# Performance work log

Measured on AMD Instinct MI355X. Metric: run time of the kernel, lower is better.

The kernel has to match this reference:

```python
import jax, jax.numpy as jnp
import numpy as np

B, T, V, H = 128, 256, 512, 1024
EOS_ID = 1


def _onehot_seq(key, eos_pos):
    k1, = jax.random.split(key, 1)
    toks = jax.random.randint(k1, (B, T), 2, V)  # avoid 0/1 so EOS only where planted
    toks = toks.at[jnp.arange(B), eos_pos].set(EOS_ID)
    return jax.nn.one_hot(toks, V, dtype=jnp.float32)


def setup_inputs() -> dict:
    key = jax.random.key(0)
    ks = jax.random.split(key, 12)
    enc_eos = jax.random.randint(ks[0], (B,), T // 2, T)
    dec_eos = jax.random.randint(ks[1], (B,), T // 2, T)
    s = 0.05
    return {
        "encoder_inputs": _onehot_seq(ks[2], enc_eos),
        "decoder_inputs": _onehot_seq(ks[3], dec_eos),
        "enc_Wi": jax.random.normal(ks[4], (V, 4 * H), jnp.float32) * s,
        "enc_Wh": jax.random.normal(ks[5], (H, 4 * H), jnp.float32) * s,
        "enc_b": jnp.zeros((4 * H,), jnp.float32),
        "dec_Wi": jax.random.normal(ks[6], (V, 4 * H), jnp.float32) * s,
        "dec_Wh": jax.random.normal(ks[7], (H, 4 * H), jnp.float32) * s,
        "dec_b": jnp.zeros((4 * H,), jnp.float32),
        "dense_W": jax.random.normal(ks[8], (H, V), jnp.float32) * s,
        "dense_b": jnp.zeros((V,), jnp.float32),
    }


def get_sequence_lengths(seq, eos_id=EOS_ID):
    eos_row = seq[:, :, eos_id]                      # [B,T]
    eos_idx = jnp.argmax(eos_row == eos_id, axis=-1)  # first position hitting EOS
    found = eos_row[jnp.arange(seq.shape[0]), eos_idx] == eos_id
    return jnp.where(found, eos_idx + 1, seq.shape[1])


def lstm_scan(c0, h0, x_btv, Wi, Wh, b):
    """Scans an LSTM over time axis 1; returns (c_seq, h_seq) each [B,T,H]."""
    def step(carry, x):
        c, h = carry
        z = x @ Wi + h @ Wh + b                      # [B,4H]
        i, f, g, o = jnp.split(z, 4, axis=-1)
        c = jax.nn.sigmoid(f) * c + jax.nn.sigmoid(i) * jnp.tanh(g)
        h = jax.nn.sigmoid(o) * jnp.tanh(c)
        return (c, h), (c, h)
    xs = jnp.swapaxes(x_btv, 0, 1)                   # [T,B,V]
    _, (cs, hs) = jax.lax.scan(step, (c0, h0), xs)
    return jnp.swapaxes(cs, 0, 1), jnp.swapaxes(hs, 0, 1)


def reference(encoder_inputs, decoder_inputs, enc_Wi, enc_Wh, enc_b,
              dec_Wi, dec_Wh, dec_b, dense_W, dense_b):
    b = encoder_inputs.shape[0]
    # --- encoder ---
    lengths = get_sequence_lengths(encoder_inputs)
    idx = jnp.maximum(0, lengths - 1)
    c0 = jnp.zeros((b, H), encoder_inputs.dtype)
    h0 = jnp.zeros((b, H), encoder_inputs.dtype)
    cs, hs = lstm_scan(c0, h0, encoder_inputs, enc_Wi, enc_Wh, enc_b)
    ar = jnp.arange(b)
    c_enc, h_enc = cs[ar, idx], hs[ar, idx]          # carry at EOS step
    # --- decoder (teacher forcing on decoder_inputs[:, :-1]) ---
    _, hd = lstm_scan(c_enc, h_enc, decoder_inputs[:, :-1], dec_Wi, dec_Wh, dec_b)
    logits = hd @ dense_W + dense_b                  # [B,T-1,V]
    return logits
```

## Files before the change

kernel.cpp:

```cpp
#include <hip/hip_runtime.h>

#define Bv 128
#define Tv 256
#define Vv 512
#define Hv 1024
#define FH 4096
#define TD 255

typedef unsigned short ushort_t;
typedef __attribute__((ext_vector_type(8))) short bf16x8;
typedef __attribute__((ext_vector_type(4))) float f32x4;

__device__ __forceinline__ ushort_t f2bf(float f) {
    unsigned u = __float_as_uint(f);
    unsigned r = (u + 0x7fffu + ((u >> 16) & 1u)) >> 16;
    return (ushort_t)r;
}
__device__ __forceinline__ float bf2f(ushort_t h) {
    return __uint_as_float(((unsigned)h) << 16);
}
__device__ __forceinline__ float sigm(float x) {
    return 1.0f / (1.0f + expf(-x));
}

__global__ __launch_bounds__(256) void wsplit_t(
    const float* __restrict__ W, int K, int N,
    ushort_t* __restrict__ hiT, ushort_t* __restrict__ loT)
{
    __shared__ float ts[32][65];
    const int n0 = blockIdx.x * 64, k0 = blockIdx.y * 32;
    const int tid = threadIdx.x;
#pragma unroll
    for (int i = 0; i < 8; i++) {
        int f = tid + i * 256;
        int k = f >> 6, nn = f & 63;
        ts[k][nn] = W[(size_t)(k0 + k) * N + n0 + nn];
    }
    __syncthreads();
#pragma unroll
    for (int i = 0; i < 8; i++) {
        int f = tid + i * 256;
        int nn = f >> 5, k = f & 31;
        float v = ts[k][nn];
        ushort_t h = f2bf(v);
        ushort_t l = f2bf(v - bf2f(h));
        size_t o = (size_t)(n0 + nn) * K + k0 + k;
        hiT[o] = h;
        loT[o] = l;
    }
}

__global__ __launch_bounds__(256) void extract_tokens(
    const float* __restrict__ x, int* __restrict__ tok)
{
    int row = blockIdx.x * 4 + (threadIdx.x >> 6);
    int lane = threadIdx.x & 63;
    const float* p = x + (size_t)row * Vv;
    int found = -1;
#pragma unroll
    for (int i = 0; i < 8; i++)
        if (p[lane + i * 64] > 0.5f) found = lane + i * 64;
#pragma unroll
    for (int off = 32; off > 0; off >>= 1) {
        int o = __shfl_down(found, off);
        found = found > o ? found : o;
    }
    if (lane == 0) tok[row] = found;
}

__global__ void find_eos(const int* __restrict__ tok, int* __restrict__ idx)
{
    int b = threadIdx.x;
    int first = Tv - 1;
    for (int t = Tv - 1; t >= 0; t--)
        if (tok[b * Tv + t] == 1) first = t;
    idx[b] = first;
}

__global__ __launch_bounds__(1024, 4) void lstm_step(
    const ushort_t* __restrict__ WhiT, const ushort_t* __restrict__ WloT,
    const float* __restrict__ Wi,
    const float* __restrict__ bias,
    const int* __restrict__ tok, int t,
    const ushort_t* __restrict__ hin_hi, const ushort_t* __restrict__ hin_lo,
    ushort_t* __restrict__ hout_hi, ushort_t* __restrict__ hout_lo,
    float* __restrict__ c_state,
    ushort_t* __restrict__ hex_hi, ushort_t* __restrict__ hex_lo,
    const int* __restrict__ save_idx,
    float* __restrict__ c_save, ushort_t* __restrict__ hs_hi, ushort_t* __restrict__ hs_lo)
{
    __shared__ float z_s[4][32][68];
    const int tid = threadIdx.x;
    const int wave = tid >> 6, lane = tid & 63;
    const int wk = wave >> 2;
    const int wm = wave & 1, wn = (wave >> 1) & 1;
    const int n = lane & 15, quad = lane >> 4;
    const int j0 = blockIdx.x * 16;
    const int b0 = blockIdx.y * 32;
    const int k0 = wk * 256;

    const bool act = tid < 512;
    const int bl = tid >> 4, jl = tid & 15;
    const int b_e = b0 + bl, col = j0 + jl;
    float w0 = 0.f, w1 = 0.f, w2 = 0.f, w3 = 0.f;
    float bz0 = 0.f, bz1 = 0.f, bz2 = 0.f, bz3 = 0.f;
    float c_old = 0.f;
    int sidx = -1;
    size_t off = 0;
    if (act) {
        int tk = tok[b_e * Tv + t];
        const float* wr = Wi + (size_t)tk * FH + col;
        w0 = wr[0]; w1 = wr[Hv]; w2 = wr[2 * Hv]; w3 = wr[3 * Hv];
        bz0 = bias[col];          bz1 = bias[Hv + col];
        bz2 = bias[2 * Hv + col]; bz3 = bias[3 * Hv + col];
        off = (size_t)b_e * Hv + col;
        c_old = c_state[off];
        if (save_idx) sidx = save_idx[b_e];
    }

    const size_t arow = (size_t)(b0 + wm * 16 + n) * Hv + k0 + quad * 8;
    const size_t g0 = (size_t)((2 * wn + 0) * Hv + j0 + n) * Hv + k0 + quad * 8;
    const size_t g1 = (size_t)((2 * wn + 1) * Hv + j0 + n) * Hv + k0 + quad * 8;

    f32x4 acc0 = {0.f, 0.f, 0.f, 0.f}, acc1 = {0.f, 0.f, 0.f, 0.f};

#pragma unroll 2
    for (int kc = 0; kc < 256; kc += 32) {
        bf16x8 ahi = *(const bf16x8*)(hin_hi + arow + kc);
        bf16x8 alo = *(const bf16x8*)(hin_lo + arow + kc);
        bf16x8 b0h = *(const bf16x8*)(WhiT + g0 + kc);
        bf16x8 b0l = *(const bf16x8*)(WloT + g0 + kc);
        bf16x8 b1h = *(const bf16x8*)(WhiT + g1 + kc);
        bf16x8 b1l = *(const bf16x8*)(WloT + g1 + kc);
        acc0 = __builtin_amdgcn_mfma_f32_16x16x32_bf16(ahi, b0h, acc0, 0, 0, 0);
        acc1 = __builtin_amdgcn_mfma_f32_16x16x32_bf16(ahi, b1h, acc1, 0, 0, 0);
        acc0 = __builtin_amdgcn_mfma_f32_16x16x32_bf16(alo, b0h, acc0, 0, 0, 0);
        acc1 = __builtin_amdgcn_mfma_f32_16x16x32_bf16(alo, b1h, acc1, 0, 0, 0);
        acc0 = __builtin_amdgcn_mfma_f32_16x16x32_bf16(ahi, b0l, acc0, 0, 0, 0);
        acc1 = __builtin_amdgcn_mfma_f32_16x16x32_bf16(ahi, b1l, acc1, 0, 0, 0);
    }

    const int row0 = wm * 16 + quad * 4;
    const int cb0 = (2 * wn + 0) * 16 + n;
    const int cb1 = cb0 + 16;
#pragma unroll
    for (int r = 0; r < 4; r++) {
        z_s[wk][row0 + r][cb0] = acc0[r];
        z_s[wk][row0 + r][cb1] = acc1[r];
    }
    __syncthreads();

    if (act) {
        float z0 = bz0 + w0, z1 = bz1 + w1, z2 = bz2 + w2, z3 = bz3 + w3;
#pragma unroll
        for (int q = 0; q < 4; q++) {
            z0 += z_s[q][bl][jl];
            z1 += z_s[q][bl][16 + jl];
            z2 += z_s[q][bl][32 + jl];
            z3 += z_s[q][bl][48 + jl];
        }
        float si = sigm(z0), sf = sigm(z1), so = sigm(z3);
        float gg = tanhf(z2);
        float cn = sf * c_old + si * gg;
        float hn = so * tanhf(cn);
        c_state[off] = cn;
        ushort_t hh = f2bf(hn);
        ushort_t hl = f2bf(hn - bf2f(hh));
        hout_hi[off] = hh;
        hout_lo[off] = hl;
        if (hex_hi) { hex_hi[off] = hh; hex_lo[off] = hl; }
        if (save_idx) {
            if (t == sidx) { c_save[off] = cn; hs_hi[off] = hh; hs_lo[off] = hl; }
        }
    }
}

__global__ __launch_bounds__(256) void dense_mfma(
    const ushort_t* __restrict__ Ahi, const ushort_t* __restrict__ Alo,
    const ushort_t* __restrict__ WhiT, const ushort_t* __restrict__ WloT,
    const float* __restrict__ bias, float* __restrict__ out)
{
    const int tid = threadIdx.x;
    const int wave = tid >> 6, lane = tid & 63;
    const int wm = wave & 1, wn = wave >> 1;
    const int n = lane & 15, quad = lane >> 4;
    const int m0 = blockIdx.y * 32 + wm * 16;
    const int c0 = blockIdx.x * 64 + wn * 32;

    const size_t arow = (size_t)(m0 + n) * Hv + quad * 8;
    const size_t g0 = (size_t)(c0 + 0 + n) * Hv + quad * 8;
    const size_t g1 = (size_t)(c0 + 16 + n) * Hv + quad * 8;

    f32x4 acc0 = {0.f, 0.f, 0.f, 0.f}, acc1 = {0.f, 0.f, 0.f, 0.f};

#pragma unroll 2
    for (int kc = 0; kc < Hv; kc += 32) {
        bf16x8 ahi = *(const bf16x8*)(Ahi + arow + kc);
        bf16x8 alo = *(const bf16x8*)(Alo + arow + kc);
        bf16x8 b0h = *(const bf16x8*)(WhiT + g0 + kc);
        bf16x8 b0l = *(const bf16x8*)(WloT + g0 + kc);
        bf16x8 b1h = *(const bf16x8*)(WhiT + g1 + kc);
        bf16x8 b1l = *(const bf16x8*)(WloT + g1 + kc);
        acc0 = __builtin_amdgcn_mfma_f32_16x16x32_bf16(ahi, b0h, acc0, 0, 0, 0);
        acc1 = __builtin_amdgcn_mfma_f32_16x16x32_bf16(ahi, b1h, acc1, 0, 0, 0);
        acc0 = __builtin_amdgcn_mfma_f32_16x16x32_bf16(alo, b0h, acc0, 0, 0, 0);
        acc1 = __builtin_amdgcn_mfma_f32_16x16x32_bf16(alo, b1h, acc1, 0, 0, 0);
        acc0 = __builtin_amdgcn_mfma_f32_16x16x32_bf16(ahi, b0l, acc0, 0, 0, 0);
        acc1 = __builtin_amdgcn_mfma_f32_16x16x32_bf16(ahi, b1l, acc1, 0, 0, 0);
    }

#pragma unroll
    for (int r = 0; r < 4; r++) {
        int row = m0 + quad * 4 + r;
        int tt = row >> 7, bb = row & 127;
        size_t o = ((size_t)bb * TD + tt) * Vv;
        int col0 = c0 + n, col1 = c0 + 16 + n;
        out[o + col0] = acc0[r] + bias[col0];
        out[o + col1] = acc1[r] + bias[col1];
    }
}

extern "C" void kernel_launch(void* const* d_in, const int* in_sizes, int n_in,
                              void* d_out, int out_size, void* d_ws, size_t ws_size,
                              hipStream_t stream)
{
    const float* enc_in  = (const float*)d_in[0];
    const float* dec_in  = (const float*)d_in[1];
    const float* enc_Wi  = (const float*)d_in[2];
    const float* enc_Wh  = (const float*)d_in[3];
    const float* enc_b   = (const float*)d_in[4];
    const float* dec_Wi  = (const float*)d_in[5];
    const float* dec_Wh  = (const float*)d_in[6];
    const float* dec_b   = (const float*)d_in[7];
    const float* dense_W = (const float*)d_in[8];
    const float* dense_b = (const float*)d_in[9];
    float* out = (float*)d_out;

    char* wp = (char*)d_ws;
    auto take = [&](size_t bytes) -> char* {
        char* p = wp;
        wp += (bytes + 255) & ~(size_t)255;
        return p;
    };

    ushort_t* hd_hi = (ushort_t*)take((size_t)TD * Bv * Hv * 2);
    ushort_t* hd_lo = (ushort_t*)take((size_t)TD * Bv * Hv * 2);
    ushort_t* eWhi  = (ushort_t*)take((size_t)FH * Hv * 2);
    ushort_t* eWlo  = (ushort_t*)take((size_t)FH * Hv * 2);
    ushort_t* dWhi  = (ushort_t*)take((size_t)FH * Hv * 2);
    ushort_t* dWlo  = (ushort_t*)take((size_t)FH * Hv * 2);
    ushort_t* nWhi  = (ushort_t*)take((size_t)Vv * Hv * 2);
    ushort_t* nWlo  = (ushort_t*)take((size_t)Vv * Hv * 2);
    ushort_t* hbh0  = (ushort_t*)take((size_t)Bv * Hv * 2);
    ushort_t* hbl0  = (ushort_t*)take((size_t)Bv * Hv * 2);
    ushort_t* hbh1  = (ushort_t*)take((size_t)Bv * Hv * 2);
    ushort_t* hbl1  = (ushort_t*)take((size_t)Bv * Hv * 2);
    ushort_t* hshi  = (ushort_t*)take((size_t)Bv * Hv * 2);
    ushort_t* hslo  = (ushort_t*)take((size_t)Bv * Hv * 2);
    float*    c_state = (float*)take((size_t)Bv * Hv * 4);
    float*    c_save  = (float*)take((size_t)Bv * Hv * 4);
    int*      etok  = (int*)take((size_t)Bv * Tv * 4);
    int*      dtok  = (int*)take((size_t)Bv * Tv * 4);
    int*      eidx  = (int*)take((size_t)Bv * 4);

    ushort_t* hbh[2] = {hbh0, hbh1};
    ushort_t* hbl[2] = {hbl0, hbl1};

    wsplit_t<<<dim3(FH / 64, Hv / 32), 256, 0, stream>>>(enc_Wh, Hv, FH, eWhi, eWlo);
    wsplit_t<<<dim3(FH / 64, Hv / 32), 256, 0, stream>>>(dec_Wh, Hv, FH, dWhi, dWlo);
    wsplit_t<<<dim3(Vv / 64, Hv / 32), 256, 0, stream>>>(dense_W, Hv, Vv, nWhi, nWlo);
    extract_tokens<<<Bv * Tv / 4, 256, 0, stream>>>(enc_in, etok);
    extract_tokens<<<Bv * Tv / 4, 256, 0, stream>>>(dec_in, dtok);
    find_eos<<<1, Bv, 0, stream>>>(etok, eidx);

    hipMemsetAsync(hbh0, 0, (size_t)Bv * Hv * 2, stream);
    hipMemsetAsync(hbl0, 0, (size_t)Bv * Hv * 2, stream);
    hipMemsetAsync(c_state, 0, (size_t)Bv * Hv * 4, stream);

    for (int t = 0; t < Tv; t++) {
        lstm_step<<<dim3(64, 4), 1024, 0, stream>>>(
            eWhi, eWlo, enc_Wi, enc_b, etok, t,
            hbh[t & 1], hbl[t & 1], hbh[(t + 1) & 1], hbl[(t + 1) & 1],
            c_state, nullptr, nullptr, eidx, c_save, hshi, hslo);
    }

    hipMemcpyAsync(c_state, c_save, (size_t)Bv * Hv * 4, hipMemcpyDeviceToDevice, stream);
    hipMemcpyAsync(hbh0, hshi, (size_t)Bv * Hv * 2, hipMemcpyDeviceToDevice, stream);
    hipMemcpyAsync(hbl0, hslo, (size_t)Bv * Hv * 2, hipMemcpyDeviceToDevice, stream);

    for (int t = 0; t < TD; t++) {
        lstm_step<<<dim3(64, 4), 1024, 0, stream>>>(
            dWhi, dWlo, dec_Wi, dec_b, dtok, t,
            hbh[t & 1], hbl[t & 1], hbh[(t + 1) & 1], hbl[(t + 1) & 1],
            c_state, hd_hi + (size_t)t * Bv * Hv, hd_lo + (size_t)t * Bv * Hv,
            nullptr, nullptr, nullptr, nullptr);
    }

    dense_mfma<<<dim3(Vv / 64, (TD * Bv) / 32), 256, 0, stream>>>(
        hd_hi, hd_lo, nWhi, nWlo, dense_b, out);
}
```

Before: 13.53 ms.

## Double batch tile per LSTM step block and prepack input weights with bias

Each lstm_step block now covers 64 batch rows instead of 32, so every wave computes a 2x2 grid of MFMA tiles and reuses each Wh fragment across two batch sub-tiles. The grid shrinks from 256 to 128 blocks and all 1024 threads take part in the gate epilogue. Input-weight rows and bias are pre-packed into an interleaved float4 layout so each thread does one vector gather per step. The three device-to-device copies between encoder and decoder are removed by feeding the saved state straight into the first decoder step. The trade-off is fewer blocks in flight on a large GPU, and the dropped occupancy hint allows higher register use per thread.

```diff
diff --git a/kernel.cpp b/kernel.cpp
--- a/kernel.cpp
+++ b/kernel.cpp
@@ -50,6 +50,19 @@
     }
 }
 
+__global__ __launch_bounds__(1024) void wi_pack(
+    const float* __restrict__ Wi, const float* __restrict__ bias,
+    float* __restrict__ Wp)
+{
+    const int v = blockIdx.x, j = threadIdx.x;
+    f32x4 o;
+    o[0] = Wi[(size_t)v * FH + j]          + bias[j];
+    o[1] = Wi[(size_t)v * FH + Hv + j]     + bias[Hv + j];
+    o[2] = Wi[(size_t)v * FH + 2 * Hv + j] + bias[2 * Hv + j];
+    o[3] = Wi[(size_t)v * FH + 3 * Hv + j] + bias[3 * Hv + j];
+    *(f32x4*)(Wp + ((size_t)v * 1024 + j) * 4) = o;
+}
+
 __global__ __launch_bounds__(256) void extract_tokens(
     const float* __restrict__ x, int* __restrict__ tok)
 {
@@ -77,81 +90,82 @@
     idx[b] = first;
 }
 
-__global__ __launch_bounds__(1024, 4) void lstm_step(
+__global__ __launch_bounds__(1024) void lstm_step(
     const ushort_t* __restrict__ WhiT, const ushort_t* __restrict__ WloT,
-    const float* __restrict__ Wi,
-    const float* __restrict__ bias,
+    const float* __restrict__ Wp,
     const int* __restrict__ tok, int t,
     const ushort_t* __restrict__ hin_hi, const ushort_t* __restrict__ hin_lo,
     ushort_t* __restrict__ hout_hi, ushort_t* __restrict__ hout_lo,
-    float* __restrict__ c_state,
+    const float* __restrict__ c_in, float* __restrict__ c_out,
     ushort_t* __restrict__ hex_hi, ushort_t* __restrict__ hex_lo,
     const int* __restrict__ save_idx,
     float* __restrict__ c_save, ushort_t* __restrict__ hs_hi, ushort_t* __restrict__ hs_lo)
 {
-    __shared__ float z_s[4][32][68];
+    __shared__ float z_s[4][64][66];
     const int tid = threadIdx.x;
     const int wave = tid >> 6, lane = tid & 63;
     const int wk = wave >> 2;
-    const int wm = wave & 1, wn = (wave >> 1) & 1;
+    const int wm = (wave >> 1) & 1;
+    const int wn = wave & 1;
     const int n = lane & 15, quad = lane >> 4;
     const int j0 = blockIdx.x * 16;
-    const int b0 = blockIdx.y * 32;
+    const int b0 = blockIdx.y * 64;
     const int k0 = wk * 256;
 
-    const bool act = tid < 512;
     const int bl = tid >> 4, jl = tid & 15;
-    const int b_e = b0 + bl, col = j0 + jl;
-    float w0 = 0.f, w1 = 0.f, w2 = 0.f, w3 = 0.f;
-    float bz0 = 0.f, bz1 = 0.f, bz2 = 0.f, bz3 = 0.f;
-    float c_old = 0.f;
-    int sidx = -1;
-    size_t off = 0;
-    if (act) {
-        int tk = tok[b_e * Tv + t];
-        const float* wr = Wi + (size_t)tk * FH + col;
-        w0 = wr[0]; w1 = wr[Hv]; w2 = wr[2 * Hv]; w3 = wr[3 * Hv];
-        bz0 = bias[col];          bz1 = bias[Hv + col];
-        bz2 = bias[2 * Hv + col]; bz3 = bias[3 * Hv + col];
-        off = (size_t)b_e * Hv + col;
-        c_old = c_state[off];
-        if (save_idx) sidx = save_idx[b_e];
-    }
-
-    const size_t arow = (size_t)(b0 + wm * 16 + n) * Hv + k0 + quad * 8;
-    const size_t g0 = (size_t)((2 * wn + 0) * Hv + j0 + n) * Hv + k0 + quad * 8;
-    const size_t g1 = (size_t)((2 * wn + 1) * Hv + j0 + n) * Hv + k0 + quad * 8;
-
-    f32x4 acc0 = {0.f, 0.f, 0.f, 0.f}, acc1 = {0.f, 0.f, 0.f, 0.f};
+    const int b_e = b0 + bl, j = j0 + jl;
+    const int tk = tok[b_e * Tv + t];
+    const f32x4 wv = *(const f32x4*)(Wp + ((size_t)tk * 1024 + j) * 4);
+    const size_t off = (size_t)b_e * Hv + j;
+    const float c_old = c_in[off];
+    const int sidx = save_idx ? save_idx[b_e] : -1;
+
+    const size_t a0 = (size_t)(b0 + wm * 32 + n) * Hv + k0 + quad * 8;
+    const size_t a1 = a0 + (size_t)16 * Hv;
+    const size_t g0 = (size_t)((wn * 2 + 0) * Hv + j0 + n) * Hv + k0 + quad * 8;
+    const size_t g1 = (size_t)((wn * 2 + 1) * Hv + j0 + n) * Hv + k0 + quad * 8;
+
+    f32x4 acc00 = {0,0,0,0}, acc01 = {0,0,0,0}, acc10 = {0,0,0,0}, acc11 = {0,0,0,0};
 
 #pragma unroll 2
     for (int kc = 0; kc < 256; kc += 32) {
-        bf16x8 ahi = *(const bf16x8*)(hin_hi + arow + kc);
-        bf16x8 alo = *(const bf16x8*)(hin_lo + arow + kc);
+        bf16x8 a0h = *(const bf16x8*)(hin_hi + a0 + kc);
+        bf16x8 a0l = *(const bf16x8*)(hin_lo + a0 + kc);
+        bf16x8 a1h = *(const bf16x8*)(hin_hi + a1 + kc);
+        bf16x8 a1l = *(const bf16x8*)(hin_lo + a1 + kc);
         bf16x8 b0h = *(const bf16x8*)(WhiT + g0 + kc);
         bf16x8 b0l = *(const bf16x8*)(WloT + g0 + kc);
         bf16x8 b1h = *(const bf16x8*)(WhiT + g1 + kc);
         bf16x8 b1l = *(const bf16x8*)(WloT + g1 + kc);
-        acc0 = __builtin_amdgcn_mfma_f32_16x16x32_bf16(ahi, b0h, acc0, 0, 0, 0);
-        acc1 = __builtin_amdgcn_mfma_f32_16x16x32_bf16(ahi, b1h, acc1, 0, 0, 0);
-        acc0 = __builtin_amdgcn_mfma_f32_16x16x32_bf16(alo, b0h, acc0, 0, 0, 0);
-        acc1 = __builtin_amdgcn_mfma_f32_16x16x32_bf16(alo, b1h, acc1, 0, 0, 0);
-        acc0 = __builtin_amdgcn_mfma_f32_16x16x32_bf16(ahi, b0l, acc0, 0, 0, 0);
-        acc1 = __builtin_amdgcn_mfma_f32_16x16x32_bf16(ahi, b1l, acc1, 0, 0, 0);
-    }
-
-    const int row0 = wm * 16 + quad * 4;
-    const int cb0 = (2 * wn + 0) * 16 + n;
-    const int cb1 = cb0 + 16;
-#pragma unroll
-    for (int r = 0; r < 4; r++) {
-        z_s[wk][row0 + r][cb0] = acc0[r];
-        z_s[wk][row0 + r][cb1] = acc1[r];
+        acc00 = __builtin_amdgcn_mfma_f32_16x16x32_bf16(a0h, b0h, acc00, 0, 0, 0);
+        acc01 = __builtin_amdgcn_mfma_f32_16x16x32_bf16(a0h, b1h, acc01, 0, 0, 0);
+        acc10 = __builtin_amdgcn_mfma_f32_16x16x32_bf16(a1h, b0h, acc10, 0, 0, 0);
+        acc11 = __builtin_amdgcn_mfma_f32_16x16x32_bf16(a1h, b1h, acc11, 0, 0, 0);
+        acc00 = __builtin_amdgcn_mfma_f32_16x16x32_bf16(a0l, b0h, acc00, 0, 0, 0);
+        acc01 = __builtin_amdgcn_mfma_f32_16x16x32_bf16(a0l, b1h, acc01, 0, 0, 0);
+        acc10 = __builtin_amdgcn_mfma_f32_16x16x32_bf16(a1l, b0h, acc10, 0, 0, 0);
+        acc11 = __builtin_amdgcn_mfma_f32_16x16x32_bf16(a1l, b1h, acc11, 0, 0, 0);
+        acc00 = __builtin_amdgcn_mfma_f32_16x16x32_bf16(a0h, b0l, acc00, 0, 0, 0);
+        acc01 = __builtin_amdgcn_mfma_f32_16x16x32_bf16(a0h, b1l, acc01, 0, 0, 0);
+        acc10 = __builtin_amdgcn_mfma_f32_16x16x32_bf16(a1h, b0l, acc10, 0, 0, 0);
+        acc11 = __builtin_amdgcn_mfma_f32_16x16x32_bf16(a1h, b1l, acc11, 0, 0, 0);
+    }
+
+    {
+        const int rb = wm * 32 + quad * 4;
+        const int cc = wn * 32 + n;
+#pragma unroll
+        for (int r = 0; r < 4; r++) {
+            z_s[wk][rb + r][cc]           = acc00[r];
+            z_s[wk][rb + r][cc + 16]      = acc01[r];
+            z_s[wk][rb + 16 + r][cc]      = acc10[r];
+            z_s[wk][rb + 16 + r][cc + 16] = acc11[r];
+        }
     }
     __syncthreads();
 
-    if (act) {
-        float z0 = bz0 + w0, z1 = bz1 + w1, z2 = bz2 + w2, z3 = bz3 + w3;
+    {
+        float z0 = wv[0], z1 = wv[1], z2 = wv[2], z3 = wv[3];
 #pragma unroll
         for (int q = 0; q < 4; q++) {
             z0 += z_s[q][bl][jl];
@@ -163,7 +177,7 @@
         float gg = tanhf(z2);
         float cn = sf * c_old + si * gg;
         float hn = so * tanhf(cn);
-        c_state[off] = cn;
+        c_out[off] = cn;
         ushort_t hh = f2bf(hn);
         ushort_t hl = f2bf(hn - bf2f(hh));
         hout_hi[off] = hh;
@@ -251,6 +265,8 @@
     ushort_t* dWlo  = (ushort_t*)take((size_t)FH * Hv * 2);
     ushort_t* nWhi  = (ushort_t*)take((size_t)Vv * Hv * 2);
     ushort_t* nWlo  = (ushort_t*)take((size_t)Vv * Hv * 2);
+    float*    eWp   = (float*)take((size_t)Vv * Hv * 4 * 4);
+    float*    dWp   = (float*)take((size_t)Vv * Hv * 4 * 4);
     ushort_t* hbh0  = (ushort_t*)take((size_t)Bv * Hv * 2);
     ushort_t* hbl0  = (ushort_t*)take((size_t)Bv * Hv * 2);
     ushort_t* hbh1  = (ushort_t*)take((size_t)Bv * Hv * 2);
@@ -269,6 +285,8 @@
     wsplit_t<<<dim3(FH / 64, Hv / 32), 256, 0, stream>>>(enc_Wh, Hv, FH, eWhi, eWlo);
     wsplit_t<<<dim3(FH / 64, Hv / 32), 256, 0, stream>>>(dec_Wh, Hv, FH, dWhi, dWlo);
     wsplit_t<<<dim3(Vv / 64, Hv / 32), 256, 0, stream>>>(dense_W, Hv, Vv, nWhi, nWlo);
+    wi_pack<<<dim3(Vv), 1024, 0, stream>>>(enc_Wi, enc_b, eWp);
+    wi_pack<<<dim3(Vv), 1024, 0, stream>>>(dec_Wi, dec_b, dWp);
     extract_tokens<<<Bv * Tv / 4, 256, 0, stream>>>(enc_in, etok);
     extract_tokens<<<Bv * Tv / 4, 256, 0, stream>>>(dec_in, dtok);
     find_eos<<<1, Bv, 0, stream>>>(etok, eidx);
@@ -278,21 +296,20 @@
     hipMemsetAsync(c_state, 0, (size_t)Bv * Hv * 4, stream);
 
     for (int t = 0; t < Tv; t++) {
-        lstm_step<<<dim3(64, 4), 1024, 0, stream>>>(
-            eWhi, eWlo, enc_Wi, enc_b, etok, t,
+        lstm_step<<<dim3(64, 2), 1024, 0, stream>>>(
+            eWhi, eWlo, eWp, etok, t,
             hbh[t & 1], hbl[t & 1], hbh[(t + 1) & 1], hbl[(t + 1) & 1],
-            c_state, nullptr, nullptr, eidx, c_save, hshi, hslo);
-    }
-
-    hipMemcpyAsync(c_state, c_save, (size_t)Bv * Hv * 4, hipMemcpyDeviceToDevice, stream);
-    hipMemcpyAsync(hbh0, hshi, (size_t)Bv * Hv * 2, hipMemcpyDeviceToDevice, stream);
-    hipMemcpyAsync(hbl0, hslo, (size_t)Bv * Hv * 2, hipMemcpyDeviceToDevice, stream);
+            c_state, c_state, nullptr, nullptr, eidx, c_save, hshi, hslo);
+    }
 
     for (int t = 0; t < TD; t++) {
-        lstm_step<<<dim3(64, 4), 1024, 0, stream>>>(
-            dWhi, dWlo, dec_Wi, dec_b, dtok, t,
-            hbh[t & 1], hbl[t & 1], hbh[(t + 1) & 1], hbl[(t + 1) & 1],
-            c_state, hd_hi + (size_t)t * Bv * Hv, hd_lo + (size_t)t * Bv * Hv,
+        const ushort_t* ih = (t == 0) ? hshi : hbh[t & 1];
+        const ushort_t* il = (t == 0) ? hslo : hbl[t & 1];
+        const float*    ci = (t == 0) ? c_save : c_state;
+        lstm_step<<<dim3(64, 2), 1024, 0, stream>>>(
+            dWhi, dWlo, dWp, dtok, t,
+            ih, il, hbh[(t + 1) & 1], hbl[(t + 1) & 1],
+            ci, c_state, hd_hi + (size_t)t * Bv * Hv, hd_lo + (size_t)t * Bv * Hv,
             nullptr, nullptr, nullptr, nullptr);
     }
 
```

New measurement: 17.17 ms. 1.27x slower.
